# Performance work log

Measured on AMD Instinct MI355X. Metric: run time of the kernel, lower is better.

The kernel has to match this reference:

```python
import jax, jax.numpy as jnp
import numpy as np

B, H, W = 64, 224, 224
EPS = 1e-5


def setup_inputs() -> dict:
    key = jax.random.key(0)
    ks = jax.random.split(key, 8)
    n = lambda k, s, std: jax.random.normal(k, s, jnp.float32) * std
    return {
        "x": jax.random.normal(ks[0], (B, 1, H, W), jnp.float32),
        "conv1_w": n(ks[1], (24, 1, 3, 3), 0.2),
        "conv1_b": jnp.zeros((24,), jnp.float32),
        "bn1_g": jnp.ones((24,), jnp.float32),
        "bn1_b": jnp.zeros((24,), jnp.float32),
        "conv2_w": n(ks[2], (48, 24, 3, 3), 0.07),
        "conv2_b": jnp.zeros((48,), jnp.float32),
        "bn2_g": jnp.ones((48,), jnp.float32),
        "bn2_b": jnp.zeros((48,), jnp.float32),
        "fconv_w": n(ks[3], (48, 48, 56, 56), 0.003),
        "fconv_b": jnp.zeros((48,), jnp.float32),
        "lin1_w": n(ks[4], (24, 48), 0.02),
        "lin1_b": jnp.zeros((24,), jnp.float32),
        "lin2_w": n(ks[5], (4, 24), 0.01),
        "lin2_b": jnp.array([0.0, 0.0, 1.0, 0.0], jnp.float32),  # torch init: identity transform bias
    }


def conv2d(x, w, b):
    y = jax.lax.conv_general_dilated(x, w, (1, 1), ((1, 1), (1, 1)),
                                     dimension_numbers=("NCHW", "OIHW", "NCHW"))
    return y + b[None, :, None, None]


def batchnorm(x, g, b):
    # train-mode BN: batch statistics over (N, H, W), biased variance
    m = x.mean((0, 2, 3), keepdims=True)
    v = x.var((0, 2, 3), keepdims=True)
    return (x - m) * jax.lax.rsqrt(v + EPS) * g[None, :, None, None] + b[None, :, None, None]


def maxpool2(x):
    b, c, h, w = x.shape
    return x.reshape(b, c, h // 2, 2, w // 2, 2).max(axis=(3, 5))


def affine_grid(theta, h, w):
    # theta: [B,2,3]; align_corners=False normalized coords (torch default)
    xs = (jnp.arange(w, dtype=jnp.float32) * 2 + 1) / w - 1.0
    ys = (jnp.arange(h, dtype=jnp.float32) * 2 + 1) / h - 1.0
    gx, gy = jnp.meshgrid(xs, ys)                      # [H,W] each
    base = jnp.stack([gx, gy, jnp.ones_like(gx)], -1)  # [H,W,3] (x, y, 1)
    return jnp.einsum("bij,hwj->bhwi", theta, base)    # [B,H,W,2] -> (x, y)


def grid_sample(img, grid):
    # bilinear, zeros padding, align_corners=False (torch defaults)
    b, c, h, w = img.shape
    ix = ((grid[..., 0] + 1.0) * w - 1.0) * 0.5        # [B,H,W]
    iy = ((grid[..., 1] + 1.0) * h - 1.0) * 0.5
    x0 = jnp.floor(ix); y0 = jnp.floor(iy)
    x1 = x0 + 1.0; y1 = y0 + 1.0
    wx1 = ix - x0; wx0 = 1.0 - wx1
    wy1 = iy - y0; wy0 = 1.0 - wy1
    bidx = jnp.arange(b)[:, None, None]

    def tap(xf, yf, wgt):
        valid = (xf >= 0) & (xf < w) & (yf >= 0) & (yf < h)
        xi = jnp.clip(xf, 0, w - 1).astype(jnp.int32)
        yi = jnp.clip(yf, 0, h - 1).astype(jnp.int32)
        vals = img[bidx, :, yi, xi]                    # [B,H,W,C]
        return vals * (wgt * valid)[..., None]

    out = (tap(x0, y0, wx0 * wy0) + tap(x1, y0, wx1 * wy0)
           + tap(x0, y1, wx0 * wy1) + tap(x1, y1, wx1 * wy1))
    return jnp.transpose(out, (0, 3, 1, 2))            # [B,C,H,W]


def reference(x, conv1_w, conv1_b, bn1_g, bn1_b, conv2_w, conv2_b, bn2_g, bn2_b,
              fconv_w, fconv_b, lin1_w, lin1_b, lin2_w, lin2_b):
    b, _, h, w = x.shape
    x1 = maxpool2(jax.nn.relu(batchnorm(conv2d(x, conv1_w, conv1_b), bn1_g, bn1_b)))
    x1 = maxpool2(jax.nn.relu(batchnorm(conv2d(x1, conv2_w, conv2_b), bn2_g, bn2_b)))
    # final_conv with kernel 56 over a 56x56 map == full contraction
    feat = jnp.einsum("bchw,ochw->bo", x1, fconv_w) + fconv_b      # [B,48]
    theta4 = jax.nn.relu(feat @ lin1_w.T + lin1_b) @ lin2_w.T + lin2_b  # [B,4]
    tx, ty, scale, angle = theta4[:, 0], theta4[:, 1], theta4[:, 2], theta4[:, 3]
    c, s = jnp.cos(angle), jnp.sin(angle)
    # (T @ R @ S)[:, :2] built directly, fully vectorized over batch
    row0 = jnp.stack([scale * c, -scale * s, tx], -1)
    row1 = jnp.stack([scale * s, scale * c, ty], -1)
    theta = jnp.stack([row0, row1], 1)                 # [B,2,3]
    grid = affine_grid(theta, h, w)
    out = grid_sample(x, grid)
    return out, tx, ty, scale, angle
```

## Files before the change

### kernel.cpp

```cpp
#include <hip/hip_runtime.h>
#include <hip/hip_bf16.h>

#define NB 64
#define H0 224
#define W0 224
#define C1 24
#define C2 48
#define H1 112
#define W1 112
#define H2 56
#define W2 56
#define EPSV 1e-5f

#define WS_STATS1   0
#define WS_STATS2   432
#define WS_FEAT     1296
#define WS_B2       4368
#define WS_X2       11280
#define WS_FWT      (WS_X2 + 4818944)
#define WS_X1       9645072
#define WS_NEED_BIG ((size_t)(WS_X1 + 9633792) * 4)
#define OUT0_ELEMS  (NB*H0*W0)

typedef _Float16 v8h __attribute__((ext_vector_type(8)));
typedef float    v4f __attribute__((ext_vector_type(4)));

static __device__ __forceinline__ unsigned short f2h(float v) {
    _Float16 h = (_Float16)v;
    unsigned short us;
    __builtin_memcpy(&us, &h, 2);
    return us;
}

__global__ __launch_bounds__(256) void k_initprep(
    const float* __restrict__ w2, const float* __restrict__ fw,
    float* __restrict__ ws, _Float16* __restrict__ fwt)
{
    __shared__ _Float16 T[48][520];
    const int tid = threadIdx.x;
    const int bx = blockIdx.x;

    if (bx < 54) {
        int t = bx * 256 + tid;
        if (t < WS_B2) ws[t] = 0.f;
        if (t < 13824) {
            int e = t & 7;
            int l = (t >> 3) & 63;
            int g = t >> 9;
            int q = l >> 4, ml = l & 15;
            int kp = g / 3, nt = g % 3;
            int ic = q * 8 + e;
            int oc = nt * 16 + ml;
            float v = (ic < C1) ? w2[(oc * C1 + ic) * 9 + kp] : 0.f;
            ((_Float16*)(ws + WS_B2))[t] = (_Float16)v;
        }
    }

    const int kb = bx * 512;
#pragma unroll
    for (int t3 = 0; t3 < 24; t3++) {
        int li = tid + 256 * t3;
        int o = li / 128, k4 = li % 128;
        float4 v = *(const float4*)&fw[(long)o * 150528 + kb + 4 * k4];
        T[o][4 * k4 + 0] = (_Float16)v.x;
        T[o][4 * k4 + 1] = (_Float16)v.y;
        T[o][4 * k4 + 2] = (_Float16)v.z;
        T[o][4 * k4 + 3] = (_Float16)v.w;
    }
    __syncthreads();
    uint4* dst = (uint4*)&fwt[(long)kb * 48];
#pragma unroll
    for (int t3 = 0; t3 < 12; t3++) {
        int u = tid + 256 * t3;
        int gg = u / 384;
        int rem = u % 384;
        int o = rem / 8;
        int k8 = (rem % 8) * 8;
        dst[u] = *(const uint4*)&T[o][gg * 64 + k8];
    }
}

__global__ __launch_bounds__(256) void k_conv1_pool_stats4(
    const float* __restrict__ x, const float* __restrict__ w1, const float* __restrict__ b1,
    float* __restrict__ ws, _Float16* __restrict__ x1g)
{
    __shared__ float xt[34][36];
    __shared__ unsigned int outt[256][13];
    __shared__ float sred[2 * C1];

    const int tid = threadIdx.x;
    const int b = blockIdx.z;
    const int py0 = blockIdx.y * 16, px0 = blockIdx.x * 16;
    const int iy0 = 2 * py0 - 1, ix0 = 2 * px0 - 1;
    const float* xb = x + b * (H0 * W0);

    for (int li = tid; li < 34 * 34; li += 256) {
        int ry = li / 34, rx = li % 34;
        int gy = iy0 + ry, gx = ix0 + rx;
        bool ok = (gy >= 0) & (gy < H0) & (gx >= 0) & (gx < W0);
        xt[ry][rx] = ok ? xb[gy * W0 + gx] : 0.f;
    }

    const int wid = tid >> 6;
    const int lane = tid & 63;
    const int c0 = wid * 6;

    const int c0s = __builtin_amdgcn_readfirstlane(c0);
    const float* __restrict__ wps = w1 + c0s * 9;
    float wr[54], br[6];
#pragma unroll
    for (int k = 0; k < 54; k++) wr[k] = wps[k];
#pragma unroll
    for (int c = 0; c < 6; c++) br[c] = b1[c0s + c];

    __syncthreads();

    float s[6] = {0.f, 0.f, 0.f, 0.f, 0.f, 0.f};
    float q[6] = {0.f, 0.f, 0.f, 0.f, 0.f, 0.f};
    const int pc = lane & 15;
    const int pr0 = lane >> 4;

#pragma unroll
    for (int pp = 0; pp < 4; pp++) {
        const int pr = pr0 + 4 * pp;
        float patch[16];
#pragma unroll
        for (int i2 = 0; i2 < 4; i2++)
#pragma unroll
            for (int j2 = 0; j2 < 4; j2++)
                patch[i2 * 4 + j2] = xt[2 * pr + i2][2 * pc + j2];

        unsigned int pk[3];
#pragma unroll
        for (int cp = 0; cp < 3; cp++) {
            unsigned int pv = 0;
#pragma unroll
            for (int h = 0; h < 2; h++) {
                int c = 2 * cp + h;
                float m4 = -1e30f;
#pragma unroll
                for (int sy = 0; sy < 2; sy++)
#pragma unroll
                    for (int sx = 0; sx < 2; sx++) {
                        float a = br[c];
#pragma unroll
                        for (int ky = 0; ky < 3; ky++)
#pragma unroll
                            for (int kx = 0; kx < 3; kx++)
                                a = fmaf(patch[(sy + ky) * 4 + (sx + kx)], wr[c * 9 + ky * 3 + kx], a);
                        s[c] += a;
                        q[c] = fmaf(a, a, q[c]);
                        m4 = fmaxf(m4, a);
                    }
                pv |= ((unsigned int)f2h(m4)) << (16 * h);
            }
            pk[cp] = pv;
        }
        int pos = pr * 16 + pc;
        outt[pos][wid * 3 + 0] = pk[0];
        outt[pos][wid * 3 + 1] = pk[1];
        outt[pos][wid * 3 + 2] = pk[2];
    }

#pragma unroll
    for (int c = 0; c < 6; c++) {
#pragma unroll
        for (int off = 32; off > 0; off >>= 1) {
            s[c] += __shfl_down(s[c], off, 64);
            q[c] += __shfl_down(q[c], off, 64);
        }
    }
    if (lane == 0) {
#pragma unroll
        for (int c = 0; c < 6; c++) {
            sred[c0 + c] = s[c];
            sred[C1 + c0 + c] = q[c];
        }
    }
    __syncthreads();

    if (tid < 2 * C1) {
        int cp = (blockIdx.x + 7 * blockIdx.y + 49 * blockIdx.z) & 7;
        atomicAdd(&ws[WS_STATS1 + cp * 2 * C1 + tid], sred[tid]);
    }

    for (int u = tid; u < 768; u += 256) {
        int pos = u / 3, prt = u % 3;
        int pr = pos >> 4, pcc = pos & 15;
        long p = (long)(b * H1 + (py0 + pr)) * W1 + (px0 + pcc);
        uint4 v;
        v.x = outt[pos][4 * prt + 0];
        v.y = outt[pos][4 * prt + 1];
        v.z = outt[pos][4 * prt + 2];
        v.w = outt[pos][4 * prt + 3];
        *(uint4*)(x1g + p * C1 + prt * 8) = v;
    }
}

__global__ __launch_bounds__(256, 2) void k_conv2_fused5(
    const _Float16* __restrict__ x1g, const _Float16* __restrict__ bpp,
    const float* __restrict__ g1, const float* __restrict__ bb1,
    const float* __restrict__ b2,
    float* __restrict__ ws, unsigned int* __restrict__ pooltu)
{
    __shared__ __align__(16) _Float16 x1t[2][10][18][32];
    __shared__ float alds[C1], bflds[C1];
    __shared__ float sred[2 * C2];

    const int tid = threadIdx.x;
    const int w = tid >> 6;
    const int lane = tid & 63;
    const int ml = lane & 15;
    const int qq = lane >> 4;

    v8h B[9][3];
#pragma unroll
    for (int kp = 0; kp < 9; kp++)
#pragma unroll
        for (int nt = 0; nt < 3; nt++)
            B[kp][nt] = *(const v8h*)&bpp[((kp * 3 + nt) * 64 + lane) * 8];

    if (tid < C1) {
        float s = 0.f, q = 0.f;
#pragma unroll
        for (int i = 0; i < 8; i++) {
            s += ws[WS_STATS1 + i * 2 * C1 + tid];
            q += ws[WS_STATS1 + i * 2 * C1 + C1 + tid];
        }
        const float N = (float)(NB * H0 * W0);
        float m = s / N;
        float v = q / N - m * m;
        float a = g1[tid] / sqrtf(v + EPSV);
        alds[tid] = a;
        bflds[tid] = bb1[tid] - m * a;
    }
    if (tid < 2 * C2) sred[tid] = 0.f;

    float bias[3] = {b2[ml], b2[16 + ml], b2[32 + ml]};

    int spart[3], spr[3], spc[3]; bool swrite[3];
#pragma unroll
    for (int it3 = 0; it3 < 3; it3++) {
        int li = tid + it3 * 256;
        swrite[it3] = li < 720;
        spart[it3] = li & 3;
        int pos = li >> 2;
        spr[it3] = pos / 18;
        spc[it3] = pos % 18;
    }

    const int nb = gridDim.x;
    const int NTILE = 6272;
    int qn = NTILE / nb, rn = NTILE % nb;
    int start = (blockIdx.x < rn) ? blockIdx.x * (qn + 1)
                                  : rn * (qn + 1) + (blockIdx.x - rn) * qn;
    int cnt = (blockIdx.x < rn) ? qn + 1 : qn;

    float svacc[3] = {0.f, 0.f, 0.f}, qvacc[3] = {0.f, 0.f, 0.f};

    v8h raw[3];
    bool inb_n[3];
    {
        int t = start;
        int tb = t / 98, rem = t % 98;
        int ty = (rem / 7) * 8, txx = (rem % 7) * 16;
#pragma unroll
        for (int it3 = 0; it3 < 3; it3++) {
#pragma unroll
            for (int e = 0; e < 8; e++) raw[it3][e] = (_Float16)0.f;
            int gy = ty - 1 + spr[it3], gx = txx - 1 + spc[it3];
            inb_n[it3] = swrite[it3] & (spart[it3] < 3) &
                         (gy >= 0) & (gy < H1) & (gx >= 0) & (gx < W1);
            if (inb_n[it3])
                raw[it3] = *(const v8h*)&x1g[((tb * H1 + gy) * W1 + gx) * C1 + spart[it3] * 8];
        }
    }
    __syncthreads();

#pragma unroll
    for (int it3 = 0; it3 < 3; it3++) {
        if (swrite[it3]) {
            v8h r8;
            if (inb_n[it3]) {
#pragma unroll
                for (int e = 0; e < 8; e++) {
                    int c = spart[it3] * 8 + e;
                    float vv = fmaxf(fmaf((float)raw[it3][e], alds[c], bflds[c]), 0.f);
                    r8[e] = (_Float16)vv;
                }
            } else {
#pragma unroll
                for (int e = 0; e < 8; e++) r8[e] = (_Float16)0.f;
            }
            *(v8h*)&x1t[0][spr[it3]][spc[it3]][spart[it3] * 8] = r8;
        }
    }
    __syncthreads();

    for (int it = 0; it < cnt; it++) {
        const int cur = it & 1;
        const int t = start + it;
        const int tb = t / 98, rem = t % 98;
        const int ty = (rem / 7) * 8, txx = (rem % 7) * 16;

        const bool haveNext = (it + 1 < cnt);
        if (haveNext) {
            int t2 = t + 1;
            int nb2 = t2 / 98, rem2 = t2 % 98;
            int ny = (rem2 / 7) * 8, nx = (rem2 % 7) * 16;
#pragma unroll
            for (int it3 = 0; it3 < 3; it3++) {
#pragma unroll
                for (int e = 0; e < 8; e++) raw[it3][e] = (_Float16)0.f;
                int gy = ny - 1 + spr[it3], gx = nx - 1 + spc[it3];
                inb_n[it3] = swrite[it3] & (spart[it3] < 3) &
                             (gy >= 0) & (gy < H1) & (gx >= 0) & (gx < W1);
                if (inb_n[it3])
                    raw[it3] = *(const v8h*)&x1g[((nb2 * H1 + gy) * W1 + gx) * C1 + spart[it3] * 8];
            }
        }

        v4f acc[2][3];
#pragma unroll
        for (int mt = 0; mt < 2; mt++)
#pragma unroll
            for (int nt = 0; nt < 3; nt++)
                acc[mt][nt] = (v4f){0.f, 0.f, 0.f, 0.f};

#pragma unroll
        for (int kp = 0; kp < 9; kp++) {
            const int ky = kp / 3, kx = kp % 3;
#pragma unroll
            for (int mt = 0; mt < 2; mt++) {
                const int r = 2 * w + mt;
                v8h a = *(const v8h*)&x1t[cur][r + ky][ml + kx][qq * 8];
                acc[mt][0] = __builtin_amdgcn_mfma_f32_16x16x32_f16(a, B[kp][0], acc[mt][0], 0, 0, 0);
                acc[mt][1] = __builtin_amdgcn_mfma_f32_16x16x32_f16(a, B[kp][1], acc[mt][1], 0, 0, 0);
                acc[mt][2] = __builtin_amdgcn_mfma_f32_16x16x32_f16(a, B[kp][2], acc[mt][2], 0, 0, 0);
            }
        }

#pragma unroll
        for (int nt = 0; nt < 3; nt++) {
            int oc = nt * 16 + ml;
            float z[2][4];
#pragma unroll
            for (int mt = 0; mt < 2; mt++)
#pragma unroll
                for (int rg = 0; rg < 4; rg++) {
                    float val = acc[mt][nt][rg] + bias[nt];
                    z[mt][rg] = val;
                    svacc[nt] += val;
                    qvacc[nt] = fmaf(val, val, qvacc[nt]);
                }
            int py = (ty >> 1) + w;
            float m0 = fmaxf(fmaxf(z[0][0], z[0][1]), fmaxf(z[1][0], z[1][1]));
            float m1 = fmaxf(fmaxf(z[0][2], z[0][3]), fmaxf(z[1][2], z[1][3]));
            int px0 = (txx >> 1) + qq * 2;
            int k = oc * 3136 + py * W2 + px0;
            unsigned int pk2 = (unsigned int)f2h(m0) | ((unsigned int)f2h(m1) << 16);
            pooltu[(((k >> 6) * NB + tb) << 5) + ((k & 63) >> 1)] = pk2;
        }

        if (haveNext) {
#pragma unroll
            for (int it3 = 0; it3 < 3; it3++) {
                if (swrite[it3]) {
                    v8h r8;
                    if (inb_n[it3]) {
#pragma unroll
                        for (int e = 0; e < 8; e++) {
                            int c = spart[it3] * 8 + e;
                            float vv = fmaxf(fmaf((float)raw[it3][e], alds[c], bflds[c]), 0.f);
                            r8[e] = (_Float16)vv;
                        }
                    } else {
#pragma unroll
                        for (int e = 0; e < 8; e++) r8[e] = (_Float16)0.f;
                    }
                    *(v8h*)&x1t[cur ^ 1][spr[it3]][spc[it3]][spart[it3] * 8] = r8;
                }
            }
        }
        __syncthreads();
    }

#pragma unroll
    for (int nt = 0; nt < 3; nt++) {
        float sv = svacc[nt], qv = qvacc[nt];
        sv += __shfl_xor(sv, 16, 64); qv += __shfl_xor(qv, 16, 64);
        sv += __shfl_xor(sv, 32, 64); qv += __shfl_xor(qv, 32, 64);
        if (qq == 0) {
            atomicAdd(&sred[nt * 16 + ml], sv);
            atomicAdd(&sred[C2 + nt * 16 + ml], qv);
        }
    }
    __syncthreads();
    if (tid < 2 * C2) {
        atomicAdd(&ws[WS_STATS2 + (blockIdx.x & 7) * 2 * C2 + tid], sred[tid]);
    }
}

__global__ __launch_bounds__(256) void k_fconv6(
    const unsigned int* __restrict__ pooltu, const _Float16* __restrict__ fwt,
    const float* __restrict__ ws, const float* __restrict__ g2, const float* __restrict__ bb2,
    float* __restrict__ feat)
{
    __shared__ __align__(16) _Float16 fwh[48][136];
    __shared__ __align__(16) _Float16 x2h[64][136];
    __shared__ float csh[2 * C2];

    const int tid = threadIdx.x;
    const int bx = blockIdx.x;

    const uint4* fsrc = (const uint4*)fwt + (long)bx * 768;
    const uint4* psrc = (const uint4*)pooltu + (long)bx * 1024;
    uint4 fr[3], pr[4];
#pragma unroll
    for (int t3 = 0; t3 < 3; t3++) fr[t3] = fsrc[tid + 256 * t3];
#pragma unroll
    for (int t4 = 0; t4 < 4; t4++) pr[t4] = psrc[tid + 256 * t4];

    if (tid < C2) {
        int c = tid;
        float s = 0.f, q = 0.f;
#pragma unroll
        for (int i = 0; i < 8; i++) {
            s += ws[WS_STATS2 + i * 2 * C2 + c];
            q += ws[WS_STATS2 + i * 2 * C2 + C2 + c];
        }
        const float N = (float)(NB * H1 * W1);
        float m = s / N;
        float v = q / N - m * m;
        float a = g2[c] / sqrtf(v + EPSV);
        csh[c] = a;
        csh[C2 + c] = bb2[c] - m * a;
    }
    __syncthreads();

#pragma unroll
    for (int t3 = 0; t3 < 3; t3++) {
        int li = tid + 256 * t3;
        int gg = li / 384;
        int o = (li % 384) / 8;
        int kin = (li & 7) * 8;
        *(uint4*)&fwh[o][gg * 64 + kin] = fr[t3];
    }
    const int c0 = (2 * bx) / 49, c1 = (2 * bx + 1) / 49;
    const float a0 = csh[c0], bf0 = csh[C2 + c0];
    const float a1 = csh[c1], bf1 = csh[C2 + c1];
#pragma unroll
    for (int t4 = 0; t4 < 4; t4++) {
        int li = tid + 256 * t4;
        int gg = li >> 9;
        int b = (li & 511) >> 3;
        int kin = (li & 7) * 8;
        float aa = gg ? a1 : a0;
        float bb = gg ? bf1 : bf0;
        union { uint4 u; v8h h; } cv;
        cv.u = pr[t4];
        v8h r8;
#pragma unroll
        for (int e = 0; e < 8; e++)
            r8[e] = (_Float16)fmaxf(fmaf((float)cv.h[e], aa, bb), 0.f);
        *(v8h*)&x2h[b][gg * 64 + kin] = r8;
    }
    __syncthreads();

    const int w = tid >> 6;
    const int lane = tid & 63;
    const int ml = lane & 15;
    const int qq = lane >> 4;

    v4f acc[3];
#pragma unroll
    for (int ot = 0; ot < 3; ot++) acc[ot] = (v4f){0.f, 0.f, 0.f, 0.f};

#pragma unroll
    for (int ks = 0; ks < 4; ks++) {
        v8h a = *(const v8h*)&x2h[w * 16 + ml][ks * 32 + qq * 8];
#pragma unroll
        for (int ot = 0; ot < 3; ot++) {
            v8h bb = *(const v8h*)&fwh[ot * 16 + ml][ks * 32 + qq * 8];
            acc[ot] = __builtin_amdgcn_mfma_f32_16x16x32_f16(a, bb, acc[ot], 0, 0, 0);
        }
    }

#pragma unroll
    for (int ot = 0; ot < 3; ot++)
#pragma unroll
        for (int rg = 0; rg < 4; rg++)
            atomicAdd(&feat[(w * 16 + qq * 4 + rg) * C2 + ot * 16 + ml], acc[ot][rg]);
}

__global__ __launch_bounds__(64) void k_theta2(
    const float* __restrict__ feat, const float* __restrict__ fcb,
    const float* __restrict__ l1w, const float* __restrict__ l1b,
    const float* __restrict__ l2w, const float* __restrict__ l2b,
    float* __restrict__ tmat, float* __restrict__ out)
{
    const int b = threadIdx.x;
    float f[C2];
#pragma unroll
    for (int o = 0; o < C2; o++) f[o] = feat[b * C2 + o] + fcb[o];
    float h[24];
#pragma unroll
    for (int jj = 0; jj < 24; jj++) {
        float a = l1b[jj];
#pragma unroll
        for (int o = 0; o < C2; o++) a = fmaf(f[o], l1w[jj * C2 + o], a);
        h[jj] = fmaxf(a, 0.f);
    }
    float th[4];
#pragma unroll
    for (int k = 0; k < 4; k++) {
        float a = l2b[k];
#pragma unroll
        for (int jj = 0; jj < 24; jj++) a = fmaf(h[jj], l2w[k * 24 + jj], a);
        th[k] = a;
        out[OUT0_ELEMS + k * NB + b] = a;
    }
    float sc = th[2], an = th[3];
    float cc = cosf(an), ss = sinf(an);
    tmat[0 * NB + b] = sc * cc;
    tmat[1 * NB + b] = -sc * ss;
    tmat[2 * NB + b] = sc * ss;
    tmat[3 * NB + b] = sc * cc;
    tmat[4 * NB + b] = th[0];
    tmat[5 * NB + b] = th[1];
}

__global__ __launch_bounds__(256) void k_sample3(
    const float* __restrict__ x, const float* __restrict__ tmat, float* __restrict__ out)
{
    const int b = blockIdx.y;
    const float t00 = tmat[0 * NB + b], t01 = tmat[1 * NB + b];
    const float t10 = tmat[2 * NB + b], t11 = tmat[3 * NB + b];
    const float tx  = tmat[4 * NB + b], ty  = tmat[5 * NB + b];
    const float* xb = x + b * (H0 * W0);

    int idx = (blockIdx.x * 256 + threadIdx.x) * 2;
    int i = idx / W0, j = idx % W0;
    float ys = (2.f * (float)i + 1.f) / (float)H0 - 1.f;

    float o2[2];
#pragma unroll
    for (int px = 0; px < 2; px++) {
        float xs = (2.f * (float)(j + px) + 1.f) / (float)W0 - 1.f;
        float gx = t00 * xs + t01 * ys + tx;
        float gy = t10 * xs + t11 * ys + ty;
        float ix = ((gx + 1.f) * (float)W0 - 1.f) * 0.5f;
        float iy = ((gy + 1.f) * (float)H0 - 1.f) * 0.5f;
        float x0 = floorf(ix), y0 = floorf(iy);
        float x1f = x0 + 1.f, y1f = y0 + 1.f;
        float wx1 = ix - x0, wx0 = 1.f - wx1;
        float wy1 = iy - y0, wy0 = 1.f - wy1;
        auto tap = [&](float xf, float yf, float wgt) -> float {
            bool valid = (xf >= 0.f) & (xf < (float)W0) & (yf >= 0.f) & (yf < (float)H0);
            int xi = (int)fminf(fmaxf(xf, 0.f), (float)(W0 - 1));
            int yi = (int)fminf(fmaxf(yf, 0.f), (float)(H0 - 1));
            return valid ? xb[yi * W0 + xi] * wgt : 0.f;
        };
        o2[px] = tap(x0, y0, wx0 * wy0) + tap(x1f, y0, wx1 * wy0)
               + tap(x0, y1f, wx0 * wy1) + tap(x1f, y1f, wx1 * wy1);
    }
    *(float2*)&out[(b * H0 + i) * W0 + j] = make_float2(o2[0], o2[1]);
}

__global__ __launch_bounds__(256) void k_init(const float* __restrict__ w2, float* __restrict__ ws)
{
    int t = blockIdx.x * 256 + threadIdx.x;
    if (t < WS_B2) ws[t] = 0.f;
    if (t < 13824) {
        int e = t & 7;
        int l = (t >> 3) & 63;
        int g = t >> 9;
        int q = l >> 4, ml = l & 15;
        int kp = g / 3, nt = g % 3;
        int ic = q * 8 + e;
        int oc = nt * 16 + ml;
        float v = (ic < C1) ? w2[(oc * C1 + ic) * 9 + kp] : 0.f;
        ((_Float16*)(ws + WS_B2))[t] = (_Float16)v;
    }
}

__global__ __launch_bounds__(256) void k_conv1_stats(
    const float* __restrict__ x, const float* __restrict__ w1, const float* __restrict__ b1,
    float* __restrict__ ws)
{
    float s[C1], q[C1];
#pragma unroll
    for (int c = 0; c < C1; c++) { s[c] = 0.f; q[c] = 0.f; }
    const int NT = gridDim.x * 256;
    const int total = NB * H0 * W0;
    for (int p = blockIdx.x * 256 + threadIdx.x; p < total; p += NT) {
        int b = p / (H0 * W0);
        int r = p % (H0 * W0);
        int y = r / W0;
        int xx = r % W0;
        const float* xb = x + b * (H0 * W0);
        float patch[9];
#pragma unroll
        for (int dy = 0; dy < 3; dy++)
#pragma unroll
            for (int dx = 0; dx < 3; dx++) {
                int yy = y + dy - 1, xc = xx + dx - 1;
                bool ok = (yy >= 0) & (yy < H0) & (xc >= 0) & (xc < W0);
                patch[dy * 3 + dx] = ok ? xb[yy * W0 + xc] : 0.f;
            }
#pragma unroll
        for (int c = 0; c < C1; c++) {
            const float* wp = w1 + c * 9;
            float a = b1[c];
#pragma unroll
            for (int k = 0; k < 9; k++) a = fmaf(patch[k], wp[k], a);
            s[c] += a;
            q[c] = fmaf(a, a, q[c]);
        }
    }
#pragma unroll
    for (int c = 0; c < C1; c++) {
#pragma unroll
        for (int off = 32; off > 0; off >>= 1) {
            s[c] += __shfl_down(s[c], off, 64);
            q[c] += __shfl_down(q[c], off, 64);
        }
    }
    __shared__ float sred[2 * C1];
    if (threadIdx.x < 2 * C1) sred[threadIdx.x] = 0.f;
    __syncthreads();
    if ((threadIdx.x & 63) == 0) {
#pragma unroll
        for (int c = 0; c < C1; c++) {
            atomicAdd(&sred[c], s[c]);
            atomicAdd(&sred[C1 + c], q[c]);
        }
    }
    __syncthreads();
    if (threadIdx.x < 2 * C1) {
        atomicAdd(&ws[WS_STATS1 + (blockIdx.x & 7) * 2 * C1 + threadIdx.x], sred[threadIdx.x]);
    }
}

__global__ __launch_bounds__(256, 2) void k_conv2_fused(
    const float* __restrict__ x, const float* __restrict__ w1, const float* __restrict__ b1,
    const float* __restrict__ g1, const float* __restrict__ bb1,
    const _Float16* __restrict__ bpp, const float* __restrict__ b2,
    float* __restrict__ ws, float* __restrict__ pool)
{
    __shared__ float xt[22][38];
    __shared__ __align__(16) _Float16 x1t[10][18][32];
    __shared__ __align__(16) _Float16 Blds[13824];
    __shared__ float wlds[C1 * 9];
    __shared__ float blds[C1], alds[C1], bflds[C1];
    __shared__ float sred[2 * C2];

    const int tid = threadIdx.x;
    const int b = blockIdx.z;
    const int y0 = blockIdx.y * 8;
    const int x0 = blockIdx.x * 16;
    const float* xb = x + b * (H0 * W0);

    for (int li = tid; li < 13824 / 8; li += 256)
        ((uint4*)Blds)[li] = ((const uint4*)bpp)[li];

    if (tid < C1 * 9) wlds[tid] = w1[tid];
    if (tid < C1) {
        float s = 0.f, q = 0.f;
#pragma unroll
        for (int i = 0; i < 8; i++) {
            s += ws[WS_STATS1 + i * 2 * C1 + tid];
            q += ws[WS_STATS1 + i * 2 * C1 + C1 + tid];
        }
        const float N = (float)(NB * H0 * W0);
        float m = s / N;
        float v = q / N - m * m;
        float a = g1[tid] / sqrtf(v + EPSV);
        blds[tid] = b1[tid];
        alds[tid] = a;
        bflds[tid] = bb1[tid] - m * a;
    }
    if (tid < 2 * C2) sred[tid] = 0.f;

    const int oy0 = 2 * y0 - 3, ox0 = 2 * x0 - 3;
    for (int li = tid; li < 22 * 38; li += 256) {
        int ry = li / 38, rx = li % 38;
        int gy = oy0 + ry, gx = ox0 + rx;
        bool ok = (gy >= 0) & (gy < H0) & (gx >= 0) & (gx < W0);
        xt[ry][rx] = ok ? xb[gy * W0 + gx] : 0.f;
    }
    __syncthreads();

    if (tid < 180) {
        int pr = tid / 18, pc = tid % 18;
        int gy = y0 - 1 + pr, gx = x0 - 1 + pc;
        bool valid = (gy >= 0) & (gy < H1) & (gx >= 0) & (gx < W1);
        float patch[16];
#pragma unroll
        for (int dy = 0; dy < 4; dy++)
#pragma unroll
            for (int dx = 0; dx < 4; dx++)
                patch[dy * 4 + dx] = xt[2 * pr + dy][2 * pc + dx];
        unsigned int* dst = (unsigned int*)&x1t[pr][pc][0];
#pragma unroll
        for (int cp = 0; cp < 12; cp++) {
            unsigned int pk = 0;
#pragma unroll
            for (int h = 0; h < 2; h++) {
                int c = 2 * cp + h;
                float m4 = -1e30f;
#pragma unroll
                for (int py = 0; py < 2; py++)
#pragma unroll
                    for (int px = 0; px < 2; px++) {
                        float a = blds[c];
#pragma unroll
                        for (int ky = 0; ky < 3; ky++)
#pragma unroll
                            for (int kx = 0; kx < 3; kx++)
                                a = fmaf(patch[(py + ky) * 4 + (px + kx)], wlds[c * 9 + ky * 3 + kx], a);
                        m4 = fmaxf(m4, fmaf(a, alds[c], bflds[c]));
                    }
                float v = valid ? fmaxf(m4, 0.f) : 0.f;
                pk |= ((unsigned int)f2h(v)) << (16 * h);
            }
            dst[cp] = pk;
        }
        dst[12] = 0; dst[13] = 0; dst[14] = 0; dst[15] = 0;
    }
    __syncthreads();

    const int w = tid >> 6;
    const int lane = tid & 63;
    const int ml = lane & 15;
    const int q = lane >> 4;

    v4f acc[2][3];
#pragma unroll
    for (int mt = 0; mt < 2; mt++)
#pragma unroll
        for (int nt = 0; nt < 3; nt++)
            acc[mt][nt] = (v4f){0.f, 0.f, 0.f, 0.f};

#pragma unroll
    for (int kp = 0; kp < 9; kp++) {
        const int ky = kp / 3, kx = kp % 3;
        v8h B0 = *(const v8h*)&Blds[((kp * 3 + 0) * 64 + lane) * 8];
        v8h B1 = *(const v8h*)&Blds[((kp * 3 + 1) * 64 + lane) * 8];
        v8h B2 = *(const v8h*)&Blds[((kp * 3 + 2) * 64 + lane) * 8];
#pragma unroll
        for (int mt = 0; mt < 2; mt++) {
            const int r = 2 * w + mt;
            v8h a = *(const v8h*)&x1t[r + ky][ml + kx][q * 8];
            acc[mt][0] = __builtin_amdgcn_mfma_f32_16x16x32_f16(a, B0, acc[mt][0], 0, 0, 0);
            acc[mt][1] = __builtin_amdgcn_mfma_f32_16x16x32_f16(a, B1, acc[mt][1], 0, 0, 0);
            acc[mt][2] = __builtin_amdgcn_mfma_f32_16x16x32_f16(a, B2, acc[mt][2], 0, 0, 0);
        }
    }

#pragma unroll
    for (int nt = 0; nt < 3; nt++) {
        int oc = nt * 16 + ml;
        float bias = b2[oc];
        float z[2][4];
        float sv = 0.f, qv = 0.f;
#pragma unroll
        for (int mt = 0; mt < 2; mt++)
#pragma unroll
            for (int rg = 0; rg < 4; rg++) {
                float val = acc[mt][nt][rg] + bias;
                z[mt][rg] = val;
                sv += val;
                qv = fmaf(val, val, qv);
            }
        sv += __shfl_xor(sv, 16, 64); qv += __shfl_xor(qv, 16, 64);
        sv += __shfl_xor(sv, 32, 64); qv += __shfl_xor(qv, 32, 64);
        if (q == 0) { atomicAdd(&sred[oc], sv); atomicAdd(&sred[C2 + oc], qv); }

        int py = (y0 >> 1) + w;
#pragma unroll
        for (int j = 0; j < 2; j++) {
            float m = fmaxf(fmaxf(z[0][2 * j], z[0][2 * j + 1]),
                            fmaxf(z[1][2 * j], z[1][2 * j + 1]));
            int px = (x0 >> 1) + q * 2 + j;
            pool[((b * C2 + oc) * H2 + py) * W2 + px] = m;
        }
    }
    __syncthreads();
    if (tid < 2 * C2) {
        int cp = (blockIdx.x + 7 * blockIdx.y + 31 * blockIdx.z) & 7;
        atomicAdd(&ws[WS_STATS2 + cp * 2 * C2 + tid], sred[tid]);
    }
}

#define KC 512
#define KSUB 128
__global__ __launch_bounds__(256) void k_fconv(
    const float* __restrict__ pool, const float* __restrict__ ws,
    const float* __restrict__ g2, const float* __restrict__ bb2,
    const float* __restrict__ fw, float* __restrict__ feat)
{
    __shared__ float fwt[C2][KSUB + 1];
    __shared__ float x2t[NB][KSUB + 1];
    __shared__ float csh[2 * C2];
    if (threadIdx.x < C2) {
        int c = threadIdx.x;
        float s = 0.f, q = 0.f;
#pragma unroll
        for (int i = 0; i < 8; i++) {
            s += ws[WS_STATS2 + i * 2 * C2 + c];
            q += ws[WS_STATS2 + i * 2 * C2 + C2 + c];
        }
        const float N = (float)(NB * H1 * W1);
        float m = s / N;
        float v = q / N - m * m;
        float a = g2[c] / sqrtf(v + EPSV);
        csh[c] = a;
        csh[C2 + c] = bb2[c] - m * a;
    }
    int k0 = blockIdx.x * KC;
    int i = threadIdx.x / 16, j = threadIdx.x % 16;
    float acc[3][4] = {{0.f}};
    for (int sub = 0; sub < KC / KSUB; sub++) {
        int kb = k0 + sub * KSUB;
        __syncthreads();
        for (int li = threadIdx.x; li < C2 * KSUB; li += 256) {
            int o = li / KSUB, k = li % KSUB;
            fwt[o][k] = fw[o * 150528 + kb + k];
        }
        for (int li = threadIdx.x; li < NB * KSUB; li += 256) {
            int b = li / KSUB, k = li % KSUB;
            int kk = kb + k;
            int c = kk / (H2 * W2);
            float v = pool[b * 150528 + kk];
            x2t[b][k] = fmaxf(fmaf(v, csh[c], csh[C2 + c]), 0.f);
        }
        __syncthreads();
        for (int k = 0; k < KSUB; k++) {
            float fa[3], xv[4];
#pragma unroll
            for (int c = 0; c < 3; c++) fa[c] = fwt[i + 16 * c][k];
#pragma unroll
            for (int d = 0; d < 4; d++) xv[d] = x2t[j + 16 * d][k];
#pragma unroll
            for (int c = 0; c < 3; c++)
#pragma unroll
                for (int d = 0; d < 4; d++)
                    acc[c][d] = fmaf(fa[c], xv[d], acc[c][d]);
        }
    }
#pragma unroll
    for (int c = 0; c < 3; c++)
#pragma unroll
        for (int d = 0; d < 4; d++)
            atomicAdd(&feat[(j + 16 * d) * C2 + (i + 16 * c)], acc[c][d]);
}

__global__ __launch_bounds__(256) void k_sample(
    const float* __restrict__ x, const float* __restrict__ feat, const float* __restrict__ fcb,
    const float* __restrict__ l1w, const float* __restrict__ l1b,
    const float* __restrict__ l2w, const float* __restrict__ l2b,
    float* __restrict__ out)
{
    __shared__ float hsh[24];
    __shared__ float th[4];
    int b = blockIdx.y;
    int tid = threadIdx.x;
    if (tid < 24) {
        float a = l1b[tid];
        for (int o = 0; o < C2; o++)
            a = fmaf(feat[b * C2 + o] + fcb[o], l1w[tid * C2 + o], a);
        hsh[tid] = fmaxf(a, 0.f);
    }
    __syncthreads();
    if (tid < 4) {
        float a = l2b[tid];
        for (int jj = 0; jj < 24; jj++) a = fmaf(hsh[jj], l2w[tid * 24 + jj], a);
        th[tid] = a;
        if (blockIdx.x == 0) out[OUT0_ELEMS + tid * NB + b] = a;
    }
    __syncthreads();

    int idx = blockIdx.x * 256 + tid;
    int i = idx / W0, j = idx % W0;
    float tx = th[0], ty = th[1], sc = th[2], an = th[3];
    float cc = cosf(an), ss = sinf(an);
    float t00 = sc * cc, t01 = -sc * ss, t10 = sc * ss, t11 = sc * cc;
    float xs = (2.f * (float)j + 1.f) / (float)W0 - 1.f;
    float ys = (2.f * (float)i + 1.f) / (float)H0 - 1.f;
    float gx = t00 * xs + t01 * ys + tx;
    float gy = t10 * xs + t11 * ys + ty;
    float ix = ((gx + 1.f) * (float)W0 - 1.f) * 0.5f;
    float iy = ((gy + 1.f) * (float)H0 - 1.f) * 0.5f;
    float x0 = floorf(ix), y0 = floorf(iy);
    float x1f = x0 + 1.f, y1f = y0 + 1.f;
    float wx1 = ix - x0, wx0 = 1.f - wx1;
    float wy1 = iy - y0, wy0 = 1.f - wy1;
    const float* xb = x + b * (H0 * W0);
    auto tap = [&](float xf, float yf, float wgt) -> float {
        bool valid = (xf >= 0.f) & (xf < (float)W0) & (yf >= 0.f) & (yf < (float)H0);
        int xi = (int)fminf(fmaxf(xf, 0.f), (float)(W0 - 1));
        int yi = (int)fminf(fmaxf(yf, 0.f), (float)(H0 - 1));
        return valid ? xb[yi * W0 + xi] * wgt : 0.f;
    };
    float o = tap(x0, y0, wx0 * wy0) + tap(x1f, y0, wx1 * wy0)
            + tap(x0, y1f, wx0 * wy1) + tap(x1f, y1f, wx1 * wy1);
    out[(b * H0 + i) * W0 + j] = o;
}

extern "C" void kernel_launch(void* const* d_in, const int* in_sizes, int n_in,
                              void* d_out, int out_size, void* d_ws, size_t ws_size,
                              hipStream_t stream)
{
    const float* x    = (const float*)d_in[0];
    const float* c1w  = (const float*)d_in[1];
    const float* c1b  = (const float*)d_in[2];
    const float* bn1g = (const float*)d_in[3];
    const float* bn1b = (const float*)d_in[4];
    const float* c2w  = (const float*)d_in[5];
    const float* c2b  = (const float*)d_in[6];
    const float* bn2g = (const float*)d_in[7];
    const float* bn2b = (const float*)d_in[8];
    const float* fw   = (const float*)d_in[9];
    const float* fcb  = (const float*)d_in[10];
    const float* l1w  = (const float*)d_in[11];
    const float* l1b  = (const float*)d_in[12];
    const float* l2w  = (const float*)d_in[13];
    const float* l2b  = (const float*)d_in[14];
    float* ws  = (float*)d_ws;
    float* out = (float*)d_out;

    if (ws_size >= WS_NEED_BIG) {
        k_initprep<<<dim3(294), 256, 0, stream>>>(c2w, fw, ws, (_Float16*)(ws + WS_FWT));
        k_conv1_pool_stats4<<<dim3(7, 7, 64), 256, 0, stream>>>(
            x, c1w, c1b, ws, (_Float16*)(ws + WS_X1));
        k_conv2_fused5<<<dim3(512), 256, 0, stream>>>(
            (const _Float16*)(ws + WS_X1), (const _Float16*)(ws + WS_B2),
            bn1g, bn1b, c2b, ws, (unsigned int*)(ws + WS_X2));
        k_fconv6<<<dim3(1176), 256, 0, stream>>>(
            (const unsigned int*)(ws + WS_X2), (const _Float16*)(ws + WS_FWT),
            ws, bn2g, bn2b, ws + WS_FEAT);
        k_theta2<<<dim3(1), 64, 0, stream>>>(
            ws + WS_FEAT, fcb, l1w, l1b, l2w, l2b, ws + WS_B2, out);
        k_sample3<<<dim3(98, 64), 256, 0, stream>>>(x, ws + WS_B2, out);
    } else {
        k_init<<<dim3(54), 256, 0, stream>>>(c2w, ws);
        k_conv1_stats<<<dim3(1024), 256, 0, stream>>>(x, c1w, c1b, ws);
        k_conv2_fused<<<dim3(7, 14, 64), 256, 0, stream>>>(
            x, c1w, c1b, bn1g, bn1b, (const _Float16*)(ws + WS_B2), c2b, ws, ws + WS_X2);
        k_fconv<<<dim3(150528 / KC), 256, 0, stream>>>(ws + WS_X2, ws, bn2g, bn2b, fw, ws + WS_FEAT);
        k_sample<<<dim3(196, 64), 256, 0, stream>>>(x, ws + WS_FEAT, fcb, l1w, l1b, l2w, l2b, out);
    }
}
```

Measured before the change: 247.5 us.

## Merge weight prep into conv1 kernel and fold theta MLP into sampler

The fconv weight transpose/conversion and conv2 weight packing now run as extra blocks (1176 blocks of 128-column chunks) inside the conv1+pool+stats kernel, so they share one launch and can overlap. A tiny zeroing kernel clears the stats region first. The separate single-block theta kernel is removed: each sampling block recomputes the small MLP and affine matrix for its batch element. This saves launches and serial tiny-kernel latency, at the cost of redundant MLP work per block and a shared-memory union in the merged kernel.

```diff
diff --git a/kernel.cpp b/kernel.cpp
--- a/kernel.cpp
+++ b/kernel.cpp
@@ -32,65 +32,71 @@
     return us;
 }
 
-__global__ __launch_bounds__(256) void k_initprep(
+__global__ __launch_bounds__(256) void k_zero1(float* __restrict__ ws)
+{
+    int t = blockIdx.x * 256 + threadIdx.x;
+    if (t < 432) ws[t] = 0.f;
+}
+
+__global__ __launch_bounds__(256) void k_stats_prep(
+    const float* __restrict__ x, const float* __restrict__ w1, const float* __restrict__ b1,
     const float* __restrict__ w2, const float* __restrict__ fw,
-    float* __restrict__ ws, _Float16* __restrict__ fwt)
-{
-    __shared__ _Float16 T[48][520];
+    float* __restrict__ ws, _Float16* __restrict__ x1g, _Float16* __restrict__ fwt)
+{
+    __shared__ __align__(16) unsigned char smem[18432];
     const int tid = threadIdx.x;
-    const int bx = blockIdx.x;
-
-    if (bx < 54) {
-        int t = bx * 256 + tid;
-        if (t < WS_B2) ws[t] = 0.f;
-        if (t < 13824) {
-            int e = t & 7;
-            int l = (t >> 3) & 63;
-            int g = t >> 9;
-            int q = l >> 4, ml = l & 15;
-            int kp = g / 3, nt = g % 3;
-            int ic = q * 8 + e;
-            int oc = nt * 16 + ml;
-            float v = (ic < C1) ? w2[(oc * C1 + ic) * 9 + kp] : 0.f;
-            ((_Float16*)(ws + WS_B2))[t] = (_Float16)v;
-        }
-    }
-
-    const int kb = bx * 512;
-#pragma unroll
-    for (int t3 = 0; t3 < 24; t3++) {
-        int li = tid + 256 * t3;
-        int o = li / 128, k4 = li % 128;
-        float4 v = *(const float4*)&fw[(long)o * 150528 + kb + 4 * k4];
-        T[o][4 * k4 + 0] = (_Float16)v.x;
-        T[o][4 * k4 + 1] = (_Float16)v.y;
-        T[o][4 * k4 + 2] = (_Float16)v.z;
-        T[o][4 * k4 + 3] = (_Float16)v.w;
-    }
-    __syncthreads();
-    uint4* dst = (uint4*)&fwt[(long)kb * 48];
-#pragma unroll
-    for (int t3 = 0; t3 < 12; t3++) {
-        int u = tid + 256 * t3;
-        int gg = u / 384;
-        int rem = u % 384;
-        int o = rem / 8;
-        int k8 = (rem % 8) * 8;
-        dst[u] = *(const uint4*)&T[o][gg * 64 + k8];
-    }
-}
-
-__global__ __launch_bounds__(256) void k_conv1_pool_stats4(
-    const float* __restrict__ x, const float* __restrict__ w1, const float* __restrict__ b1,
-    float* __restrict__ ws, _Float16* __restrict__ x1g)
-{
-    __shared__ float xt[34][36];
-    __shared__ unsigned int outt[256][13];
-    __shared__ float sred[2 * C1];
-
-    const int tid = threadIdx.x;
-    const int b = blockIdx.z;
-    const int py0 = blockIdx.y * 16, px0 = blockIdx.x * 16;
+    const int bid = blockIdx.x;
+
+    if (bid >= 3136) {
+        _Float16 (*T)[136] = (_Float16(*)[136])smem;
+        const int p = bid - 3136;
+        if (p < 54) {
+            int t = p * 256 + tid;
+            if (t >= 432 && t < WS_B2) ws[t] = 0.f;
+            if (t < 13824) {
+                int e = t & 7;
+                int l = (t >> 3) & 63;
+                int g = t >> 9;
+                int q = l >> 4, ml = l & 15;
+                int kp = g / 3, nt = g % 3;
+                int ic = q * 8 + e;
+                int oc = nt * 16 + ml;
+                float v = (ic < C1) ? w2[(oc * C1 + ic) * 9 + kp] : 0.f;
+                ((_Float16*)(ws + WS_B2))[t] = (_Float16)v;
+            }
+        }
+        const int kb = p * 128;
+#pragma unroll
+        for (int t3 = 0; t3 < 6; t3++) {
+            int li = tid + 256 * t3;
+            int o = li >> 5, k4 = li & 31;
+            float4 v = *(const float4*)&fw[(long)o * 150528 + kb + 4 * k4];
+            T[o][4 * k4 + 0] = (_Float16)v.x;
+            T[o][4 * k4 + 1] = (_Float16)v.y;
+            T[o][4 * k4 + 2] = (_Float16)v.z;
+            T[o][4 * k4 + 3] = (_Float16)v.w;
+        }
+        __syncthreads();
+        uint4* dst = (uint4*)&fwt[(long)kb * 48];
+#pragma unroll
+        for (int t3 = 0; t3 < 3; t3++) {
+            int u = tid + 256 * t3;
+            int gg = u / 384;
+            int rem = u % 384;
+            int o = rem >> 3;
+            int k8 = (rem & 7) * 8;
+            dst[u] = *(const uint4*)&T[o][gg * 64 + k8];
+        }
+        return;
+    }
+
+    float (*xt)[36] = (float(*)[36])smem;
+    unsigned int (*outt)[13] = (unsigned int(*)[13])(smem + 4896);
+    float* sred = (float*)(smem + 18208);
+
+    const int b = bid / 49;
+    const int rem0 = bid % 49;
+    const int py0 = (rem0 / 7) * 16, px0 = (rem0 % 7) * 16;
     const int iy0 = 2 * py0 - 1, ix0 = 2 * px0 - 1;
     const float* xb = x + b * (H0 * W0);
 
@@ -180,8 +186,7 @@
     __syncthreads();
 
     if (tid < 2 * C1) {
-        int cp = (blockIdx.x + 7 * blockIdx.y + 49 * blockIdx.z) & 7;
-        atomicAdd(&ws[WS_STATS1 + cp * 2 * C1 + tid], sred[tid]);
+        atomicAdd(&ws[WS_STATS1 + (bid & 7) * 2 * C1 + tid], sred[tid]);
     }
 
     for (int u = tid; u < 768; u += 256) {
@@ -493,53 +498,39 @@
             atomicAdd(&feat[(w * 16 + qq * 4 + rg) * C2 + ot * 16 + ml], acc[ot][rg]);
 }
 
-__global__ __launch_bounds__(64) void k_theta2(
-    const float* __restrict__ feat, const float* __restrict__ fcb,
+__global__ __launch_bounds__(256) void k_sample4(
+    const float* __restrict__ x, const float* __restrict__ feat, const float* __restrict__ fcb,
     const float* __restrict__ l1w, const float* __restrict__ l1b,
     const float* __restrict__ l2w, const float* __restrict__ l2b,
-    float* __restrict__ tmat, float* __restrict__ out)
-{
-    const int b = threadIdx.x;
-    float f[C2];
-#pragma unroll
-    for (int o = 0; o < C2; o++) f[o] = feat[b * C2 + o] + fcb[o];
-    float h[24];
-#pragma unroll
-    for (int jj = 0; jj < 24; jj++) {
-        float a = l1b[jj];
-#pragma unroll
-        for (int o = 0; o < C2; o++) a = fmaf(f[o], l1w[jj * C2 + o], a);
-        h[jj] = fmaxf(a, 0.f);
-    }
-    float th[4];
-#pragma unroll
-    for (int k = 0; k < 4; k++) {
-        float a = l2b[k];
-#pragma unroll
-        for (int jj = 0; jj < 24; jj++) a = fmaf(h[jj], l2w[k * 24 + jj], a);
-        th[k] = a;
-        out[OUT0_ELEMS + k * NB + b] = a;
-    }
-    float sc = th[2], an = th[3];
-    float cc = cosf(an), ss = sinf(an);
-    tmat[0 * NB + b] = sc * cc;
-    tmat[1 * NB + b] = -sc * ss;
-    tmat[2 * NB + b] = sc * ss;
-    tmat[3 * NB + b] = sc * cc;
-    tmat[4 * NB + b] = th[0];
-    tmat[5 * NB + b] = th[1];
-}
-
-__global__ __launch_bounds__(256) void k_sample3(
-    const float* __restrict__ x, const float* __restrict__ tmat, float* __restrict__ out)
-{
+    float* __restrict__ out)
+{
+    __shared__ float hsh[24];
+    __shared__ float th[4];
     const int b = blockIdx.y;
-    const float t00 = tmat[0 * NB + b], t01 = tmat[1 * NB + b];
-    const float t10 = tmat[2 * NB + b], t11 = tmat[3 * NB + b];
-    const float tx  = tmat[4 * NB + b], ty  = tmat[5 * NB + b];
+    const int tid = threadIdx.x;
+    if (tid < 24) {
+        float a = l1b[tid];
+#pragma unroll
+        for (int o = 0; o < C2; o++)
+            a = fmaf(feat[b * C2 + o] + fcb[o], l1w[tid * C2 + o], a);
+        hsh[tid] = fmaxf(a, 0.f);
+    }
+    __syncthreads();
+    if (tid < 4) {
+        float a = l2b[tid];
+#pragma unroll
+        for (int jj = 0; jj < 24; jj++) a = fmaf(hsh[jj], l2w[tid * 24 + jj], a);
+        th[tid] = a;
+        if (blockIdx.x == 0) out[OUT0_ELEMS + tid * NB + b] = a;
+    }
+    __syncthreads();
+
+    const float tx = th[0], ty = th[1], sc = th[2], an = th[3];
+    const float cc = cosf(an), ss = sinf(an);
+    const float t00 = sc * cc, t01 = -sc * ss, t10 = sc * ss, t11 = sc * cc;
     const float* xb = x + b * (H0 * W0);
 
-    int idx = (blockIdx.x * 256 + threadIdx.x) * 2;
+    int idx = (blockIdx.x * 256 + tid) * 2;
     int i = idx / W0, j = idx % W0;
     float ys = (2.f * (float)i + 1.f) / (float)H0 - 1.f;
 
@@ -931,18 +922,17 @@
     float* out = (float*)d_out;
 
     if (ws_size >= WS_NEED_BIG) {
-        k_initprep<<<dim3(294), 256, 0, stream>>>(c2w, fw, ws, (_Float16*)(ws + WS_FWT));
-        k_conv1_pool_stats4<<<dim3(7, 7, 64), 256, 0, stream>>>(
-            x, c1w, c1b, ws, (_Float16*)(ws + WS_X1));
+        k_zero1<<<dim3(2), 256, 0, stream>>>(ws);
+        k_stats_prep<<<dim3(4312), 256, 0, stream>>>(
+            x, c1w, c1b, c2w, fw, ws, (_Float16*)(ws + WS_X1), (_Float16*)(ws + WS_FWT));
         k_conv2_fused5<<<dim3(512), 256, 0, stream>>>(
             (const _Float16*)(ws + WS_X1), (const _Float16*)(ws + WS_B2),
             bn1g, bn1b, c2b, ws, (unsigned int*)(ws + WS_X2));
         k_fconv6<<<dim3(1176), 256, 0, stream>>>(
             (const unsigned int*)(ws + WS_X2), (const _Float16*)(ws + WS_FWT),
             ws, bn2g, bn2b, ws + WS_FEAT);
-        k_theta2<<<dim3(1), 64, 0, stream>>>(
-            ws + WS_FEAT, fcb, l1w, l1b, l2w, l2b, ws + WS_B2, out);
-        k_sample3<<<dim3(98, 64), 256, 0, stream>>>(x, ws + WS_B2, out);
+        k_sample4<<<dim3(98, 64), 256, 0, stream>>>(
+            x, ws + WS_FEAT, fcb, l1w, l1b, l2w, l2b, out);
     } else {
         k_init<<<dim3(54), 256, 0, stream>>>(c2w, ws);
         k_conv1_stats<<<dim3(1024), 256, 0, stream>>>(x, c1w, c1b, ws);
```

Result: faster. 220.0 us (-11.1%).
